# Optimization experiments

Measured on AMD Instinct MI355X. Metric: run time of the kernel, lower is better.

## Reference

```python
import jax, jax.numpy as jnp
import numpy as np

N, E, G = 32768, 262144, 512
IN_DIM, HID, HEADS = 300, 128, 4
D_FUSED = HID * HEADS  # 512
L = 3


def setup_inputs() -> dict:
    key = jax.random.key(0)
    ks = jax.random.split(key, 24)
    s = 0.02
    inp = {
        "x": jax.random.normal(ks[0], (N, IN_DIM), jnp.float32),
        "edge_index": jax.random.randint(ks[1], (2, E), 0, N, jnp.int32),
        "batch": jnp.sort(jax.random.randint(ks[2], (N,), 0, G, jnp.int32)),
        "syn_w": jax.random.normal(ks[3], (IN_DIM, HID)) * s,
        "syn_b": jnp.zeros((HID,), jnp.float32),
        "ant_w": jax.random.normal(ks[4], (IN_DIM, HID)) * s,
        "ant_b": jnp.zeros((HID,), jnp.float32),
        "fusion_w": jax.random.normal(ks[5], (2 * HID, D_FUSED)) * s,
        "fusion_b": jnp.zeros((D_FUSED,), jnp.float32),
        "Wq": jax.random.normal(ks[6], (L, D_FUSED, D_FUSED)) * s,
        "bq": jnp.zeros((L, D_FUSED), jnp.float32),
        "Wk": jax.random.normal(ks[7], (L, D_FUSED, D_FUSED)) * s,
        "bk": jnp.zeros((L, D_FUSED), jnp.float32),
        "Wv": jax.random.normal(ks[8], (L, D_FUSED, D_FUSED)) * s,
        "bv": jnp.zeros((L, D_FUSED), jnp.float32),
        "Wskip": jax.random.normal(ks[9], (L, D_FUSED, D_FUSED)) * s,
        "bskip": jnp.zeros((L, D_FUSED), jnp.float32),
        "cls_w1": jax.random.normal(ks[10], (D_FUSED, HID)) * s,
        "cls_b1": jnp.zeros((HID,), jnp.float32),
        "cls_w2": jax.random.normal(ks[11], (HID, 1)) * s,
        "cls_b2": jnp.zeros((1,), jnp.float32),
    }
    return inp


def _transformer_conv(h, src, dst, Wq, bq, Wk, bk, Wv, bv, Wskip, bskip):
    # PyG TransformerConv: per-edge dot-product attention, softmax over in-neighbors of dst,
    # concat heads, plus root/skip linear (root_weight=True, concat=True, no edge_attr).
    n = h.shape[0]
    q = (h @ Wq + bq).reshape(n, HEADS, HID)
    k = (h @ Wk + bk).reshape(n, HEADS, HID)
    v = (h @ Wv + bv).reshape(n, HEADS, HID)
    scale = 1.0 / np.sqrt(HID)
    logits = jnp.einsum("ehd,ehd->eh", q[dst], k[src]) * scale  # [E, H]
    m = jax.ops.segment_max(logits, dst, num_segments=n)        # [N, H]
    e = jnp.exp(logits - m[dst])
    z = jax.ops.segment_sum(e, dst, num_segments=n)
    alpha = e / (z[dst] + 1e-16)                                # [E, H]
    msg = alpha[:, :, None] * v[src]                            # [E, H, D]
    out = jax.ops.segment_sum(msg, dst, num_segments=n).reshape(n, D_FUSED)
    return out + h @ Wskip + bskip


def reference(x, edge_index, batch, syn_w, syn_b, ant_w, ant_b, fusion_w, fusion_b,
              Wq, bq, Wk, bk, Wv, bv, Wskip, bskip, cls_w1, cls_b1, cls_w2, cls_b2):
    x_syn = jax.nn.relu(x @ syn_w + syn_b)
    x_ant = jax.nn.relu(x @ ant_w + ant_b)
    h = jnp.concatenate([x_syn, x_ant], axis=1) @ fusion_w + fusion_b  # [N, 512]
    src, dst = edge_index[0], edge_index[1]
    for l in range(L):
        h = jax.nn.relu(_transformer_conv(h, src, dst, Wq[l], bq[l], Wk[l], bk[l],
                                          Wv[l], bv[l], Wskip[l], bskip[l]))
    cnt = jax.ops.segment_sum(jnp.ones((h.shape[0],), h.dtype), batch, num_segments=G)
    pooled = jax.ops.segment_sum(h, batch, num_segments=G) / jnp.maximum(cnt, 1.0)[:, None]
    hid = jax.nn.relu(pooled @ cls_w1 + cls_b1)
    out = jax.nn.sigmoid(hid @ cls_w2 + cls_b2)
    return out.squeeze()
```

## Files before the change

kernel.cpp:

```cpp
#include <hip/hip_runtime.h>
#include <hip/hip_bf16.h>
#include <math.h>

#define N_NODES 32768
#define N_EDGES 262144
#define N_GRAPHS 512
#define IN_DIM 300
#define KPAD 320
#define HID 128
#define HEADS 4
#define D_FUSED 512
#define N_LAYERS 3

typedef __hip_bfloat16 bf16;
typedef short bf16x8 __attribute__((ext_vector_type(8)));
typedef float f32x4 __attribute__((ext_vector_type(4)));

__device__ __forceinline__ float bfs_to_f(short s)
{
    unsigned u = ((unsigned)(unsigned short)s) << 16;
    return __builtin_bit_cast(float, u);
}

__device__ __forceinline__ short f_to_bfs(float v)
{
    return (short)__builtin_bit_cast(unsigned short, __float2bfloat16(v));
}

__device__ __forceinline__ void bf8_to_f32(bf16x8 v, float* f)
{
#pragma unroll
    for (int j = 0; j < 8; ++j) f[j] = bfs_to_f(v[j]);
}

__device__ __forceinline__ void gload_lds16(const void* g, void* l)
{
    __builtin_amdgcn_global_load_lds(
        (const __attribute__((address_space(1))) void*)g,
        (__attribute__((address_space(3))) void*)l, 16, 0, 0);
}

template <int K, int ACT>
__global__ __launch_bounds__(512, 2) void mfma_gemm256(
    const bf16* __restrict__ A, int lda,
    const bf16* __restrict__ Bt,
    const float* __restrict__ bias,
    bf16* __restrict__ C0, int ldc0,
    bf16* __restrict__ C1, int ldc1, int csplit,
    int nbx)
{
    __shared__ __align__(16) char lds[131072];

    const int t = threadIdx.x;
    const int wid = t >> 6, lane = t & 63;
    const int hi = lane >> 4, li = lane & 15;
    const int wr = wid >> 2, wc = wid & 3;

    int wg = blockIdx.x;
    if ((gridDim.x & 7) == 0) {
        const int cpx = gridDim.x >> 3;
        wg = (wg & 7) * cpx + (wg >> 3);
    }
    const int mb = wg / nbx, nb = wg % nbx;
    const int brow = mb * 256, bcol = nb * 256;
    constexpr int NT = K >> 6;

    const bf16* gA[4];
    const bf16* gB[4];
    int lbA[4], lbB[4];
#pragma unroll
    for (int j = 0; j < 4; ++j) {
        const int c = j * 512 + wid * 64 + lane;
        const int row = c >> 3;
        const int colb8 = ((c & 7) ^ (row & 7)) * 8;
        gA[j] = A + (size_t)(brow + row) * lda + colb8;
        gB[j] = Bt + (size_t)(bcol + row) * K + colb8;
        lbA[j] = (j * 512 + wid * 64) * 16;
        lbB[j] = 32768 + (j * 512 + wid * 64) * 16;
    }

    f32x4 acc[8][4] = {};

    auto stage = [&](int buf, int kt) {
        const int ko = kt * 64;
#pragma unroll
        for (int j = 0; j < 4; ++j)
            gload_lds16(gA[j] + ko, lds + buf * 65536 + lbA[j]);
#pragma unroll
        for (int j = 0; j < 4; ++j)
            gload_lds16(gB[j] + ko, lds + buf * 65536 + lbB[j]);
    };

    auto compute = [&](int b) {
        const char* Ab = lds + b * 65536;
        const char* Bb = Ab + 32768;
        bf16x8 bfrag[4][2];
#pragma unroll
        for (int n = 0; n < 4; ++n)
#pragma unroll
            for (int ks = 0; ks < 2; ++ks) {
                const int row = wc * 64 + n * 16 + li;
                bfrag[n][ks] = *(const bf16x8*)(
                    Bb + row * 128 + (((ks * 4 + hi) ^ (row & 7)) << 4));
            }
#pragma unroll
        for (int p = 0; p < 4; ++p) {
            bf16x8 afrag[2][2];
#pragma unroll
            for (int mm = 0; mm < 2; ++mm)
#pragma unroll
                for (int ks = 0; ks < 2; ++ks) {
                    const int row = wr * 128 + (p * 2 + mm) * 16 + li;
                    afrag[mm][ks] = *(const bf16x8*)(
                        Ab + row * 128 + (((ks * 4 + hi) ^ (row & 7)) << 4));
                }
            __builtin_amdgcn_s_setprio(1);
#pragma unroll
            for (int ks = 0; ks < 2; ++ks)
#pragma unroll
                for (int mm = 0; mm < 2; ++mm)
#pragma unroll
                    for (int n = 0; n < 4; ++n)
                        acc[p * 2 + mm][n] = __builtin_amdgcn_mfma_f32_16x16x32_bf16(
                            afrag[mm][ks], bfrag[n][ks], acc[p * 2 + mm][n], 0, 0, 0);
            __builtin_amdgcn_s_setprio(0);
        }
    };

    stage(0, 0);
#pragma unroll
    for (int kt = 0; kt < NT - 1; ++kt) {
        const int b = kt & 1;
        stage(b ^ 1, kt + 1);
        asm volatile("s_waitcnt vmcnt(8)" ::: "memory");
        __builtin_amdgcn_s_barrier();
        compute(b);
        asm volatile("" ::: "memory");
        __builtin_amdgcn_s_barrier();
    }
    asm volatile("s_waitcnt vmcnt(0)" ::: "memory");
    __builtin_amdgcn_s_barrier();
    compute((NT - 1) & 1);

#pragma unroll
    for (int m = 0; m < 8; ++m) {
#pragma unroll
        for (int n = 0; n < 4; ++n) {
            const int col = bcol + wc * 64 + n * 16 + li;
            const float bv = bias[col];
            const bool lo = (col < csplit);
            bf16* Cd = lo ? C0 : C1;
            const int ldc = lo ? ldc0 : ldc1;
            const int cc = lo ? col : col - csplit;
#pragma unroll
            for (int r = 0; r < 4; ++r) {
                const int row = brow + wr * 128 + m * 16 + hi * 4 + r;
                float v = acc[m][n][r] + bv;
                if (ACT == 1) v = fmaxf(v, 0.f);
                Cd[(size_t)row * ldc + cc] = __float2bfloat16(v);
            }
        }
    }
}

template <int ACT>
__global__ __launch_bounds__(256) void mfma_gemm(
    const bf16* __restrict__ A, int lda,
    const bf16* __restrict__ Bt,
    const float* __restrict__ bias,
    bf16* __restrict__ C, int ldc, int K)
{
    __shared__ __align__(16) char lds[16384];
    char* As = lds;
    char* Bs = lds + 8192;

    const int t = threadIdx.x;
    const int wid = t >> 6, lane = t & 63;
    const int brow = blockIdx.x * 128;
    const int bcol = blockIdx.y * 128;
    const int wr = wid >> 1, wc = wid & 1;

    f32x4 acc[4][4] = {};

    for (int k0 = 0; k0 < K; k0 += 32) {
#pragma unroll
        for (int j = 0; j < 2; ++j) {
            const int seg = wid * 2 + j;
            const int row = seg * 16 + (lane >> 2);
            const int clin = lane & 3;
            const int clog = clin ^ ((row >> 1) & 3);
            gload_lds16(A + (size_t)(brow + row) * lda + k0 + clog * 8,
                        As + seg * 1024);
            gload_lds16(Bt + (size_t)(bcol + row) * K + k0 + clog * 8,
                        Bs + seg * 1024);
        }
        __syncthreads();

        bf16x8 af[4], bfr[4];
#pragma unroll
        for (int m = 0; m < 4; ++m) {
            const int row = wr * 64 + m * 16 + (lane & 15);
            const int cl = (lane >> 4) ^ ((row >> 1) & 3);
            af[m] = *(const bf16x8*)(As + row * 64 + cl * 16);
        }
#pragma unroll
        for (int n = 0; n < 4; ++n) {
            const int row = wc * 64 + n * 16 + (lane & 15);
            const int cl = (lane >> 4) ^ ((row >> 1) & 3);
            bfr[n] = *(const bf16x8*)(Bs + row * 64 + cl * 16);
        }
#pragma unroll
        for (int m = 0; m < 4; ++m)
#pragma unroll
            for (int n = 0; n < 4; ++n)
                acc[m][n] = __builtin_amdgcn_mfma_f32_16x16x32_bf16(
                    af[m], bfr[n], acc[m][n], 0, 0, 0);
        __syncthreads();
    }

#pragma unroll
    for (int m = 0; m < 4; ++m) {
#pragma unroll
        for (int n = 0; n < 4; ++n) {
            const int col = bcol + wc * 64 + n * 16 + (lane & 15);
            const float bv = bias[col];
#pragma unroll
            for (int r = 0; r < 4; ++r) {
                const int row = brow + wr * 64 + m * 16 + (lane >> 4) * 4 + r;
                float v = acc[m][n][r] + bv;
                if (ACT == 1) v = fmaxf(v, 0.f);
                C[(size_t)row * ldc + col] = __float2bfloat16(v);
            }
        }
    }
}

__global__ void prep_xpad_kernel(const float* __restrict__ x, bf16* __restrict__ xb)
{
    const int n = blockIdx.x, k = threadIdx.x;
    xb[(size_t)n * KPAD + k] =
        __float2bfloat16(k < IN_DIM ? x[(size_t)n * IN_DIM + k] : 0.f);
}

__global__ void prep_encw_kernel(const float* __restrict__ syn_w,
                                 const float* __restrict__ ant_w,
                                 bf16* __restrict__ wt)
{
    const int c = blockIdx.x, k = threadIdx.x;
    float v = 0.f;
    if (k < IN_DIM) v = (c < HID) ? syn_w[k * HID + c] : ant_w[k * HID + (c - HID)];
    wt[c * KPAD + k] = __float2bfloat16(v);
}

__global__ void prep_fusw_kernel(const float* __restrict__ fw, bf16* __restrict__ wt)
{
    const int c = blockIdx.x, k = threadIdx.x;
    wt[c * 256 + k] = __float2bfloat16(fw[k * D_FUSED + c]);
}

__global__ __launch_bounds__(256) void prep_combw_kernel(
    const float* __restrict__ Wskip,
    const float* __restrict__ Wq,
    const float* __restrict__ Wk,
    const float* __restrict__ Wv,
    bf16* __restrict__ wt)
{
    __shared__ float tile[32][33];
    const int blk = blockIdx.x;
    const int l = blk >> 10, rem = blk & 1023;
    const int cb = rem >> 4, kb = rem & 15;
    const int c0 = cb * 32;

    const float* mat;
    int cp0;
    if (c0 < 512) {
        mat = Wskip; cp0 = c0;
    } else {
        const int cc0 = c0 - 512;
        const int hd = cc0 / 384, r0 = cc0 % 384;
        const int sel = r0 >> 7, rr0 = r0 & 127;
        mat = (sel == 0) ? Wq : (sel == 1) ? Wk : Wv;
        cp0 = hd * 128 + rr0;
    }

    const int j = threadIdx.x & 31;
    const int i0 = threadIdx.x >> 5;
#pragma unroll
    for (int s = 0; s < 4; ++s) {
        const int i = i0 + 8 * s;
        tile[i][j] = mat[((size_t)l * 512 + kb * 32 + i) * 512 + cp0 + j];
    }
    __syncthreads();
#pragma unroll
    for (int s = 0; s < 4; ++s) {
        const int jj = i0 + 8 * s;
        wt[((size_t)l * 2048 + c0 + jj) * 512 + kb * 32 + j] =
            __float2bfloat16(tile[j][jj]);
    }
}

__global__ void prep_bias_kernel(const float* __restrict__ syn_b,
                                 const float* __restrict__ ant_b,
                                 const float* __restrict__ bskip,
                                 const float* __restrict__ bq,
                                 const float* __restrict__ bk,
                                 const float* __restrict__ bv,
                                 float* __restrict__ benc,
                                 float* __restrict__ bcomb)
{
    const int i = blockIdx.x * 256 + threadIdx.x;
    if (i < 256) benc[i] = (i < HID) ? syn_b[i] : ant_b[i - HID];
    const int j = i - 256;
    if (j >= 0 && j < 6144) {
        const int l = j >> 11, c = j & 2047;
        float v;
        if (c < 512) {
            v = bskip[l * D_FUSED + c];
        } else {
            const int cc = c - 512, hd = cc / 384, r = cc % 384;
            const int sel = r >> 7, rr = r & 127;
            const float* s = (sel == 0) ? bq : (sel == 1) ? bk : bv;
            v = s[l * D_FUSED + hd * HID + rr];
        }
        bcomb[j] = v;
    }
}

__global__ void zero_int_kernel(int* __restrict__ p, int n)
{
    int i = blockIdx.x * 256 + threadIdx.x;
    if (i < n) p[i] = 0;
}

__global__ void hist_kernel(const int* __restrict__ dst, int* __restrict__ deg, int E)
{
    int e = blockIdx.x * 256 + threadIdx.x;
    if (e < E) atomicAdd(&deg[dst[e]], 1);
}

__global__ __launch_bounds__(256) void partial_sum_kernel(const int* __restrict__ deg,
                                                          int* __restrict__ part)
{
    int v = deg[blockIdx.x * 256 + threadIdx.x];
#pragma unroll
    for (int o = 32; o; o >>= 1) v += __shfl_xor(v, o);
    __shared__ int w4[4];
    if ((threadIdx.x & 63) == 0) w4[threadIdx.x >> 6] = v;
    __syncthreads();
    if (threadIdx.x == 0) part[blockIdx.x] = w4[0] + w4[1] + w4[2] + w4[3];
}

__global__ __launch_bounds__(128) void scan_part_kernel(int* __restrict__ part)
{
    __shared__ int s[128];
    const int t = threadIdx.x;
    s[t] = part[t];
    __syncthreads();
    for (int o = 1; o < 128; o <<= 1) {
        int v = (t >= o) ? s[t - o] : 0;
        __syncthreads();
        s[t] += v;
        __syncthreads();
    }
    part[t] = (t == 0) ? 0 : s[t - 1];
}

__global__ __launch_bounds__(256) void off_kernel(const int* __restrict__ deg,
                                                  const int* __restrict__ part,
                                                  int* __restrict__ off)
{
    __shared__ int s[256];
    const int b = blockIdx.x, t = threadIdx.x;
    s[t] = deg[b * 256 + t];
    __syncthreads();
    for (int o = 1; o < 256; o <<= 1) {
        int v = (t >= o) ? s[t - o] : 0;
        __syncthreads();
        s[t] += v;
        __syncthreads();
    }
    const int excl = (t == 0) ? 0 : s[t - 1];
    off[b * 256 + t] = part[b] + excl;
    if (b == 127 && t == 255) off[N_NODES] = part[127] + s[255];
}

__global__ void scatter_kernel(const int* __restrict__ src, const int* __restrict__ dst,
                               const int* __restrict__ off, int* __restrict__ cursor,
                               int* __restrict__ csr_src, int E)
{
    int e = blockIdx.x * 256 + threadIdx.x;
    if (e < E) {
        int d = dst[e];
        int pos = atomicAdd(&cursor[d], 1);
        csr_src[off[d] + pos] = src[e];
    }
}

__global__ __launch_bounds__(256) void attn_kernel(
    const bf16* __restrict__ qkv, bf16* __restrict__ hout,
    const int* __restrict__ off, const int* __restrict__ csr)
{
    const int n = blockIdx.x;
    const int hd = threadIdx.x >> 6;
    const int lane = threadIdx.x & 63;
    const int g = lane >> 4, sub = lane & 15;
    const float scale = 0.08838834764831845f;

    const bf16* qrow = qkv + (size_t)n * 1536 + hd * 384;
    float qf[8];
    bf8_to_f32(*(const bf16x8*)(qrow + sub * 8), qf);

    float m = -1e30f, z = 0.f;
    float acc[8] = {};

    const int s0 = off[n], s1 = off[n + 1];
    for (int e0 = s0; e0 < s1; e0 += 4) {
        const int e = e0 + g;
        const bool valid = (e < s1);
        const int srcn = valid ? csr[e] : 0;
        const bf16* kp = qkv + (size_t)srcn * 1536 + hd * 384 + 128;

        float kf[8];
        bf8_to_f32(*(const bf16x8*)(kp + sub * 8), kf);
        float d = 0.f;
#pragma unroll
        for (int j = 0; j < 8; ++j) d = fmaf(qf[j], kf[j], d);
        d += __shfl_xor(d, 1);
        d += __shfl_xor(d, 2);
        d += __shfl_xor(d, 4);
        d += __shfl_xor(d, 8);

        const float logit = d * scale;
        const float mn = valid ? fmaxf(m, logit) : m;
        const float corr = __expf(m - mn);
        const float w = valid ? __expf(logit - mn) : 0.f;
        z = z * corr + w;

        float vf[8];
        bf8_to_f32(*(const bf16x8*)(kp + 128 + sub * 8), vf);
#pragma unroll
        for (int j = 0; j < 8; ++j) acc[j] = acc[j] * corr + w * vf[j];
        m = mn;
    }

    float mm = fmaxf(m, __shfl_xor(m, 16));
    mm = fmaxf(mm, __shfl_xor(mm, 32));
    const float f = __expf(m - mm);
    float zz = z * f;
    zz += __shfl_xor(zz, 16);
    zz += __shfl_xor(zz, 32);
    const float inv = 1.f / (zz + 1e-16f);

    float o[8];
#pragma unroll
    for (int j = 0; j < 8; ++j) {
        float a = acc[j] * f;
        a += __shfl_xor(a, 16);
        a += __shfl_xor(a, 32);
        o[j] = a * inv;
    }

    if (g == 0) {
        const size_t ob = (size_t)n * D_FUSED + hd * HID + sub * 8;
        const bf16x8 sk = *(const bf16x8*)(hout + ob);
        bf16x8 res;
#pragma unroll
        for (int j = 0; j < 8; ++j)
            res[j] = f_to_bfs(fmaxf(o[j] + bfs_to_f(sk[j]), 0.f));
        *(bf16x8*)(hout + ob) = res;
    }
}

__global__ __launch_bounds__(256) void pool_kernel(const bf16* __restrict__ h,
                                                   const int* __restrict__ batch,
                                                   float* __restrict__ pooled)
{
    const int g = blockIdx.x;
    int a = 0, b = N_NODES;
    while (a < b) { int mid = (a + b) >> 1; if (batch[mid] < g) a = mid + 1; else b = mid; }
    const int start = a;
    b = N_NODES;
    while (a < b) { int mid = (a + b) >> 1; if (batch[mid] < g + 1) a = mid + 1; else b = mid; }
    const int end = a;
    const float invc = 1.f / fmaxf((float)(end - start), 1.f);

    const int t = threadIdx.x;
    float2 s = make_float2(0.f, 0.f);
    for (int nidx = start; nidx < end; ++nidx) {
        const bf16* p = h + (size_t)nidx * D_FUSED + t * 2;
        s.x += bfs_to_f(((const short*)p)[0]);
        s.y += bfs_to_f(((const short*)p)[1]);
    }
    pooled[(size_t)g * D_FUSED + t * 2]     = s.x * invc;
    pooled[(size_t)g * D_FUSED + t * 2 + 1] = s.y * invc;
}

__global__ __launch_bounds__(128) void cls_kernel(const float* __restrict__ pooled,
                                                  const float* __restrict__ w1,
                                                  const float* __restrict__ b1,
                                                  const float* __restrict__ w2,
                                                  const float* __restrict__ b2,
                                                  float* __restrict__ out)
{
    const int g = blockIdx.x;
    const int j = threadIdx.x;
    const float* p = pooled + (size_t)g * D_FUSED;
    float acc = 0.f;
    for (int i = 0; i < D_FUSED; ++i) acc += p[i] * w1[i * HID + j];
    const float hid = fmaxf(acc + b1[j], 0.f);
    float val = hid * w2[j];
#pragma unroll
    for (int o = 32; o; o >>= 1) val += __shfl_xor(val, o);
    __shared__ float ws2[2];
    if ((threadIdx.x & 63) == 0) ws2[threadIdx.x >> 6] = val;
    __syncthreads();
    if (threadIdx.x == 0) {
        const float sum = ws2[0] + ws2[1] + b2[0];
        out[g] = 1.f / (1.f + __expf(-sum));
    }
}

extern "C" void kernel_launch(void* const* d_in, const int* in_sizes, int n_in,
                              void* d_out, int out_size, void* d_ws, size_t ws_size,
                              hipStream_t stream)
{
    const float* x        = (const float*)d_in[0];
    const int*   ei       = (const int*)d_in[1];
    const int*   batch    = (const int*)d_in[2];
    const float* syn_w    = (const float*)d_in[3];
    const float* syn_b    = (const float*)d_in[4];
    const float* ant_w    = (const float*)d_in[5];
    const float* ant_b    = (const float*)d_in[6];
    const float* fusion_w = (const float*)d_in[7];
    const float* fusion_b = (const float*)d_in[8];
    const float* Wq       = (const float*)d_in[9];
    const float* bq       = (const float*)d_in[10];
    const float* Wk       = (const float*)d_in[11];
    const float* bk       = (const float*)d_in[12];
    const float* Wv       = (const float*)d_in[13];
    const float* bv       = (const float*)d_in[14];
    const float* Wskip    = (const float*)d_in[15];
    const float* bskip    = (const float*)d_in[16];
    const float* cls_w1   = (const float*)d_in[17];
    const float* cls_b1   = (const float*)d_in[18];
    const float* cls_w2   = (const float*)d_in[19];
    const float* cls_b2   = (const float*)d_in[20];

    const int* src = ei;
    const int* dst = ei + N_EDGES;

    const size_t NV = (size_t)N_NODES * D_FUSED;
    bf16* hA    = (bf16*)d_ws;
    bf16* hB    = hA + NV;
    bf16* qs    = hB + NV;
    bf16* wenc  = qs + (size_t)N_NODES * 1536;
    bf16* wfus  = wenc + 256 * KPAD;
    bf16* wcomb = wfus + 512 * 256;
    float* benc = (float*)(wcomb + (size_t)3 * 2048 * 512);
    float* bcomb = benc + 256;
    float* pooled = bcomb + 6144;
    int* deg    = (int*)(pooled + (size_t)N_GRAPHS * D_FUSED);
    int* cursor = deg + N_NODES;
    int* part   = cursor + N_NODES;
    int* off    = part + 128;
    int* csr    = off + N_NODES + 1;

    bf16* xb   = qs;
    bf16* tenc = hB;

    zero_int_kernel<<<(2 * N_NODES + 255) / 256, 256, 0, stream>>>(deg, 2 * N_NODES);
    hist_kernel<<<N_EDGES / 256, 256, 0, stream>>>(dst, deg, N_EDGES);
    partial_sum_kernel<<<128, 256, 0, stream>>>(deg, part);
    scan_part_kernel<<<1, 128, 0, stream>>>(part);
    off_kernel<<<128, 256, 0, stream>>>(deg, part, off);
    scatter_kernel<<<N_EDGES / 256, 256, 0, stream>>>(src, dst, off, cursor, csr, N_EDGES);

    prep_xpad_kernel<<<N_NODES, KPAD, 0, stream>>>(x, xb);
    prep_encw_kernel<<<256, KPAD, 0, stream>>>(syn_w, ant_w, wenc);
    prep_fusw_kernel<<<512, 256, 0, stream>>>(fusion_w, wfus);
    prep_combw_kernel<<<3072, 256, 0, stream>>>(Wskip, Wq, Wk, Wv, wcomb);
    prep_bias_kernel<<<25, 256, 0, stream>>>(syn_b, ant_b, bskip, bq, bk, bv, benc, bcomb);

    mfma_gemm<1><<<dim3(N_NODES / 128, 2), 256, 0, stream>>>(
        xb, KPAD, wenc, benc, tenc, 256, KPAD);
    mfma_gemm256<256, 0><<<256, 512, 0, stream>>>(
        tenc, 256, wfus, fusion_b, hA, D_FUSED, hA, D_FUSED, D_FUSED, 2);

    bf16* hcur = hA;
    bf16* hnew = hB;
    for (int l = 0; l < N_LAYERS; ++l) {
        mfma_gemm256<512, 0><<<1024, 512, 0, stream>>>(
            hcur, D_FUSED, wcomb + (size_t)l * 2048 * D_FUSED,
            bcomb + (size_t)l * 2048,
            hnew, D_FUSED, qs, 1536, 512, 8);
        attn_kernel<<<N_NODES, 256, 0, stream>>>(qs, hnew, off, csr);
        bf16* tmp = hcur; hcur = hnew; hnew = tmp;
    }

    pool_kernel<<<N_GRAPHS, 256, 0, stream>>>(hcur, batch, pooled);
    cls_kernel<<<N_GRAPHS, 128, 0, stream>>>(pooled, cls_w1, cls_b1, cls_w2, cls_b2,
                                             (float*)d_out);
}
```

Baseline: 635.8 us.

## Store K and V in FP8 and regroup QKV output into separate buffers

The fused projection GEMM now writes Q as bf16 into its own buffer and K/V as FP8 e4m3 into a separate node-major buffer, with the weight and bias column order reorganised to match. The attention kernel gathers K and V at one byte per element and converts them with packed fp8-to-f32 instructions, aiming to halve gather traffic over edges. In exchange, K and V lose precision, which may hurt accuracy, and the epilogue does more byte-sized scattered stores.

```diff
diff --git a/kernel.cpp b/kernel.cpp
--- a/kernel.cpp
+++ b/kernel.cpp
@@ -1,5 +1,6 @@
 #include <hip/hip_runtime.h>
 #include <hip/hip_bf16.h>
+#include <hip/hip_fp8.h>
 #include <math.h>
 
 #define N_NODES 32768
@@ -15,6 +16,7 @@
 typedef __hip_bfloat16 bf16;
 typedef short bf16x8 __attribute__((ext_vector_type(8)));
 typedef float f32x4 __attribute__((ext_vector_type(4)));
+typedef float f32x2 __attribute__((ext_vector_type(2)));
 
 __device__ __forceinline__ float bfs_to_f(short s)
 {
@@ -31,6 +33,32 @@
 {
 #pragma unroll
     for (int j = 0; j < 8; ++j) f[j] = bfs_to_f(v[j]);
+}
+
+__device__ __forceinline__ unsigned char f32_to_fp8(float v)
+{
+    __hip_fp8_e4m3 t(v);
+    return (unsigned char)t.__x;
+}
+
+__device__ __forceinline__ void fp8x8_to_f32(uint2 w, float* f)
+{
+#if __has_builtin(__builtin_amdgcn_cvt_pk_f32_fp8)
+    f32x2 a = __builtin_amdgcn_cvt_pk_f32_fp8((int)w.x, false);
+    f32x2 b = __builtin_amdgcn_cvt_pk_f32_fp8((int)w.x, true);
+    f32x2 c = __builtin_amdgcn_cvt_pk_f32_fp8((int)w.y, false);
+    f32x2 d = __builtin_amdgcn_cvt_pk_f32_fp8((int)w.y, true);
+    f[0] = a.x; f[1] = a.y; f[2] = b.x; f[3] = b.y;
+    f[4] = c.x; f[5] = c.y; f[6] = d.x; f[7] = d.y;
+#else
+    const unsigned char* p = (const unsigned char*)&w;
+#pragma unroll
+    for (int j = 0; j < 8; ++j) {
+        __hip_fp8_e4m3 t;
+        t.__x = (__hip_fp8_storage_t)p[j];
+        f[j] = (float)t;
+    }
+#endif
 }
 
 __device__ __forceinline__ void gload_lds16(const void* g, void* l)
@@ -40,13 +68,14 @@
         (__attribute__((address_space(3))) void*)l, 16, 0, 0);
 }
 
-template <int K, int ACT>
+template <int K, int ACT, int EPI>
 __global__ __launch_bounds__(512, 2) void mfma_gemm256(
     const bf16* __restrict__ A, int lda,
     const bf16* __restrict__ Bt,
     const float* __restrict__ bias,
     bf16* __restrict__ C0, int ldc0,
     bf16* __restrict__ C1, int ldc1, int csplit,
+    unsigned char* __restrict__ C2,
     int nbx)
 {
     __shared__ __align__(16) char lds[131072];
@@ -148,16 +177,31 @@
         for (int n = 0; n < 4; ++n) {
             const int col = bcol + wc * 64 + n * 16 + li;
             const float bv = bias[col];
-            const bool lo = (col < csplit);
-            bf16* Cd = lo ? C0 : C1;
-            const int ldc = lo ? ldc0 : ldc1;
-            const int cc = lo ? col : col - csplit;
-#pragma unroll
-            for (int r = 0; r < 4; ++r) {
-                const int row = brow + wr * 128 + m * 16 + hi * 4 + r;
-                float v = acc[m][n][r] + bv;
-                if (ACT == 1) v = fmaxf(v, 0.f);
-                Cd[(size_t)row * ldc + cc] = __float2bfloat16(v);
+            if (EPI == 0) {
+                const bool lo = (col < csplit);
+                bf16* Cd = lo ? C0 : C1;
+                const int ldc = lo ? ldc0 : ldc1;
+                const int cc = lo ? col : col - csplit;
+#pragma unroll
+                for (int r = 0; r < 4; ++r) {
+                    const int row = brow + wr * 128 + m * 16 + hi * 4 + r;
+                    float v = acc[m][n][r] + bv;
+                    if (ACT == 1) v = fmaxf(v, 0.f);
+                    Cd[(size_t)row * ldc + cc] = __float2bfloat16(v);
+                }
+            } else {
+#pragma unroll
+                for (int r = 0; r < 4; ++r) {
+                    const int row = brow + wr * 128 + m * 16 + hi * 4 + r;
+                    const float v = acc[m][n][r] + bv;
+                    if (col < 512) {
+                        C0[(size_t)row * ldc0 + col] = __float2bfloat16(v);
+                    } else if (col < 1024) {
+                        C1[(size_t)row * ldc1 + (col - 512)] = __float2bfloat16(v);
+                    } else {
+                        C2[(size_t)row * 1024 + (col - 1024)] = f32_to_fp8(v);
+                    }
+                }
             }
         }
     }
@@ -271,17 +315,9 @@
     const int cb = rem >> 4, kb = rem & 15;
     const int c0 = cb * 32;
 
-    const float* mat;
-    int cp0;
-    if (c0 < 512) {
-        mat = Wskip; cp0 = c0;
-    } else {
-        const int cc0 = c0 - 512;
-        const int hd = cc0 / 384, r0 = cc0 % 384;
-        const int sel = r0 >> 7, rr0 = r0 & 127;
-        mat = (sel == 0) ? Wq : (sel == 1) ? Wk : Wv;
-        cp0 = hd * 128 + rr0;
-    }
+    const int sel = c0 >> 9;
+    const float* mat = (sel == 0) ? Wskip : (sel == 1) ? Wq : (sel == 2) ? Wk : Wv;
+    const int cp0 = c0 & 511;
 
     const int j = threadIdx.x & 31;
     const int i0 = threadIdx.x >> 5;
@@ -313,16 +349,9 @@
     const int j = i - 256;
     if (j >= 0 && j < 6144) {
         const int l = j >> 11, c = j & 2047;
-        float v;
-        if (c < 512) {
-            v = bskip[l * D_FUSED + c];
-        } else {
-            const int cc = c - 512, hd = cc / 384, r = cc % 384;
-            const int sel = r >> 7, rr = r & 127;
-            const float* s = (sel == 0) ? bq : (sel == 1) ? bk : bv;
-            v = s[l * D_FUSED + hd * HID + rr];
-        }
-        bcomb[j] = v;
+        const int sel = c >> 9, col = c & 511;
+        const float* s = (sel == 0) ? bskip : (sel == 1) ? bq : (sel == 2) ? bk : bv;
+        bcomb[j] = s[l * D_FUSED + col];
     }
 }
 
@@ -397,8 +426,9 @@
 }
 
 __global__ __launch_bounds__(256) void attn_kernel(
-    const bf16* __restrict__ qkv, bf16* __restrict__ hout,
-    const int* __restrict__ off, const int* __restrict__ csr)
+    const bf16* __restrict__ qb, const unsigned char* __restrict__ kvb,
+    bf16* __restrict__ hout, const int* __restrict__ off,
+    const int* __restrict__ csr)
 {
     const int n = blockIdx.x;
     const int hd = threadIdx.x >> 6;
@@ -406,9 +436,8 @@
     const int g = lane >> 4, sub = lane & 15;
     const float scale = 0.08838834764831845f;
 
-    const bf16* qrow = qkv + (size_t)n * 1536 + hd * 384;
     float qf[8];
-    bf8_to_f32(*(const bf16x8*)(qrow + sub * 8), qf);
+    bf8_to_f32(*(const bf16x8*)(qb + (size_t)n * 512 + hd * 128 + sub * 8), qf);
 
     float m = -1e30f, z = 0.f;
     float acc[8] = {};
@@ -418,10 +447,10 @@
         const int e = e0 + g;
         const bool valid = (e < s1);
         const int srcn = valid ? csr[e] : 0;
-        const bf16* kp = qkv + (size_t)srcn * 1536 + hd * 384 + 128;
+        const unsigned char* kp = kvb + (size_t)srcn * 1024 + hd * 128 + sub * 8;
 
         float kf[8];
-        bf8_to_f32(*(const bf16x8*)(kp + sub * 8), kf);
+        fp8x8_to_f32(*(const uint2*)kp, kf);
         float d = 0.f;
 #pragma unroll
         for (int j = 0; j < 8; ++j) d = fmaf(qf[j], kf[j], d);
@@ -437,7 +466,7 @@
         z = z * corr + w;
 
         float vf[8];
-        bf8_to_f32(*(const bf16x8*)(kp + 128 + sub * 8), vf);
+        fp8x8_to_f32(*(const uint2*)(kp + 512), vf);
 #pragma unroll
         for (int j = 0; j < 8; ++j) acc[j] = acc[j] * corr + w * vf[j];
         m = mn;
@@ -552,8 +581,9 @@
     const size_t NV = (size_t)N_NODES * D_FUSED;
     bf16* hA    = (bf16*)d_ws;
     bf16* hB    = hA + NV;
-    bf16* qs    = hB + NV;
-    bf16* wenc  = qs + (size_t)N_NODES * 1536;
+    bf16* qbuf  = hB + NV;
+    unsigned char* kvbuf = (unsigned char*)(qbuf + NV);
+    bf16* wenc  = (bf16*)(kvbuf + (size_t)N_NODES * 1024);
     bf16* wfus  = wenc + 256 * KPAD;
     bf16* wcomb = wfus + 512 * 256;
     float* benc = (float*)(wcomb + (size_t)3 * 2048 * 512);
@@ -565,7 +595,7 @@
     int* off    = part + 128;
     int* csr    = off + N_NODES + 1;
 
-    bf16* xb   = qs;
+    bf16* xb   = qbuf;
     bf16* tenc = hB;
 
     zero_int_kernel<<<(2 * N_NODES + 255) / 256, 256, 0, stream>>>(deg, 2 * N_NODES);
@@ -583,17 +613,17 @@
 
     mfma_gemm<1><<<dim3(N_NODES / 128, 2), 256, 0, stream>>>(
         xb, KPAD, wenc, benc, tenc, 256, KPAD);
-    mfma_gemm256<256, 0><<<256, 512, 0, stream>>>(
-        tenc, 256, wfus, fusion_b, hA, D_FUSED, hA, D_FUSED, D_FUSED, 2);
+    mfma_gemm256<256, 0, 0><<<256, 512, 0, stream>>>(
+        tenc, 256, wfus, fusion_b, hA, D_FUSED, hA, D_FUSED, D_FUSED, nullptr, 2);
 
     bf16* hcur = hA;
     bf16* hnew = hB;
     for (int l = 0; l < N_LAYERS; ++l) {
-        mfma_gemm256<512, 0><<<1024, 512, 0, stream>>>(
+        mfma_gemm256<512, 0, 1><<<1024, 512, 0, stream>>>(
             hcur, D_FUSED, wcomb + (size_t)l * 2048 * D_FUSED,
             bcomb + (size_t)l * 2048,
-            hnew, D_FUSED, qs, 1536, 512, 8);
-        attn_kernel<<<N_NODES, 256, 0, stream>>>(qs, hnew, off, csr);
+            hnew, D_FUSED, qbuf, D_FUSED, 512, kvbuf, 8);
+        attn_kernel<<<N_NODES, 256, 0, stream>>>(qbuf, kvbuf, hnew, off, csr);
         bf16* tmp = hcur; hcur = hnew; hnew = tmp;
     }
 
```

After: 666.7 us. +4.9%, slower.
